# Kernel tuning notes

Hardware: AMD Instinct MI355X
Metric: run time of the kernel (lower is better)

The kernel has to match this reference:

```python
import jax, jax.numpy as jnp
import numpy as np

B, S, C, P = 1024, 336, 321, 96  # batch, seq_len, input_dim, pred_len


def setup_inputs() -> dict:
    key = jax.random.key(0)
    kx, kw, kb = jax.random.split(key, 3)
    x = jax.random.normal(kx, (B, S, C), dtype=jnp.float32)
    # per-channel Linear(seq_len -> pred_len): W[c] is [P, S], b[c] is [P]
    W = jax.random.normal(kw, (C, P, S), dtype=jnp.float32) * (1.0 / np.sqrt(S))
    b = jax.random.normal(kb, (C, P), dtype=jnp.float32) * 0.01
    return {"x": x, "W": W, "b": b}


def reference(x, W, b):
    # x: [B, S, C]
    seq_last = x[:, -1:, :]                      # [B, 1, C] (detached in torch; values identical)
    xn = x - seq_last                            # subtract last-step normalization
    # per-channel linear: out[b,c,p] = sum_s W[c,p,s] * xn[b,s,c] + b[c,p]
    out = jnp.einsum("bsc,cps->bcp", xn, W) + b  # [B, C, P]
    out = out.transpose(0, 2, 1) + seq_last      # [B, P, C], add back last value
    return out[:, :, 3]                          # [B, P], channel-3 slice
```

## Files before the change

### kernel.cpp

```cpp
#include <hip/hip_runtime.h>


constexpr int B = 1024, S = 336, C = 321, P = 96;
constexpr int BPB   = 4;
constexpr int BLOCK = 256;

__global__ __launch_bounds__(BLOCK) void nlinear_c3_kernel(
    const float* __restrict__ x, const float* __restrict__ W,
    const float* __restrict__ bias, float* __restrict__ out)
{
    __shared__ float xs[BPB][S];

    const int b0 = blockIdx.x * BPB;

    for (int idx = threadIdx.x; idx < BPB * S; idx += BLOCK) {
        const int bi = idx / S;
        const int s  = idx - bi * S;
        xs[bi][s] = x[((size_t)(b0 + bi) * S + s) * C + 3];
    }
    __syncthreads();

    const int g = threadIdx.x >> 7;
    const int p = threadIdx.x & 127;
    if (p < P) {
        const int bA = 2 * g, bB = 2 * g + 1;
        const float lastA = xs[bA][S - 1];
        const float lastB = xs[bB][S - 1];

        const float4* __restrict__ wp4 =
            reinterpret_cast<const float4*>(W + (size_t)(3 * P + p) * S);
        const float4* xA4 = reinterpret_cast<const float4*>(xs[bA]);
        const float4* xB4 = reinterpret_cast<const float4*>(xs[bB]);

        float accA = 0.f, accB = 0.f, sw = 0.f;
        #pragma unroll 4
        for (int i = 0; i < S / 4; ++i) {
            const float4 w  = wp4[i];
            const float4 a  = xA4[i];
            const float4 c  = xB4[i];
            accA += a.x * w.x + a.y * w.y + a.z * w.z + a.w * w.w;
            accB += c.x * w.x + c.y * w.y + c.z * w.z + c.w * w.w;
            sw   += w.x + w.y + w.z + w.w;
        }

        const float bb = bias[3 * P + p];
        out[(size_t)(b0 + bA) * P + p] = accA - lastA * sw + bb + lastA;
        out[(size_t)(b0 + bB) * P + p] = accB - lastB * sw + bb + lastB;
    }
}

extern "C" void kernel_launch(void* const* d_in, const int* in_sizes, int n_in,
                              void* d_out, int out_size, void* d_ws, size_t ws_size,
                              hipStream_t stream) {
    const float* x    = (const float*)d_in[0];
    const float* W    = (const float*)d_in[1];
    const float* bias = (const float*)d_in[2];
    float* out        = (float*)d_out;

    nlinear_c3_kernel<<<B / BPB, BLOCK, 0, stream>>>(x, W, bias, out);
}
```

Measured before the change: 20.66 us.

## Use one block per batch row and split the reduction over four lanes

Each block now handles a single batch row with 384 threads. Four lanes share each output p, each taking a quarter of S, and their partial sums are combined with xor shuffles. The x gather uses nontemporal loads, and launch bounds request four blocks per CU. This raises parallelism and shortens the per-thread serial chain, but W reuse across batch rows inside a block drops from four to one, so W is read from cache more often.

Result: slower. 26.52 us (+28.4%).

```diff
diff --git a/kernel.cpp b/kernel.cpp
--- a/kernel.cpp
+++ b/kernel.cpp
@@ -2,50 +2,47 @@
 
 
 constexpr int B = 1024, S = 336, C = 321, P = 96;
-constexpr int BPB   = 4;
-constexpr int BLOCK = 256;
+constexpr int BLOCK = 384;
+constexpr int QCH = S / 4;
 
-__global__ __launch_bounds__(BLOCK) void nlinear_c3_kernel(
+__global__ __launch_bounds__(BLOCK, 4) void nlinear_c3_kernel(
     const float* __restrict__ x, const float* __restrict__ W,
     const float* __restrict__ bias, float* __restrict__ out)
 {
-    __shared__ float xs[BPB][S];
+    __shared__ float xs[S];
 
-    const int b0 = blockIdx.x * BPB;
+    const int b = blockIdx.x;
+    const int t = threadIdx.x;
 
-    for (int idx = threadIdx.x; idx < BPB * S; idx += BLOCK) {
-        const int bi = idx / S;
-        const int s  = idx - bi * S;
-        xs[bi][s] = x[((size_t)(b0 + bi) * S + s) * C + 3];
+    if (t < S) {
+        xs[t] = __builtin_nontemporal_load(&x[((size_t)b * S + t) * C + 3]);
     }
     __syncthreads();
 
-    const int g = threadIdx.x >> 7;
-    const int p = threadIdx.x & 127;
-    if (p < P) {
-        const int bA = 2 * g, bB = 2 * g + 1;
-        const float lastA = xs[bA][S - 1];
-        const float lastB = xs[bB][S - 1];
+    const int p = t >> 2;
+    const int q = t & 3;
 
-        const float4* __restrict__ wp4 =
-            reinterpret_cast<const float4*>(W + (size_t)(3 * P + p) * S);
-        const float4* xA4 = reinterpret_cast<const float4*>(xs[bA]);
-        const float4* xB4 = reinterpret_cast<const float4*>(xs[bB]);
+    const float last = xs[S - 1];
 
-        float accA = 0.f, accB = 0.f, sw = 0.f;
-        #pragma unroll 4
-        for (int i = 0; i < S / 4; ++i) {
-            const float4 w  = wp4[i];
-            const float4 a  = xA4[i];
-            const float4 c  = xB4[i];
-            accA += a.x * w.x + a.y * w.y + a.z * w.z + a.w * w.w;
-            accB += c.x * w.x + c.y * w.y + c.z * w.z + c.w * w.w;
-            sw   += w.x + w.y + w.z + w.w;
-        }
+    const float4* __restrict__ wp4 =
+        reinterpret_cast<const float4*>(W + (size_t)(3 * P + p) * S + q * QCH);
+    const float4* __restrict__ xq4 =
+        reinterpret_cast<const float4*>(xs + q * QCH);
 
-        const float bb = bias[3 * P + p];
-        out[(size_t)(b0 + bA) * P + p] = accA - lastA * sw + bb + lastA;
-        out[(size_t)(b0 + bB) * P + p] = accB - lastB * sw + bb + lastB;
+    float acc = 0.f, sw = 0.f;
+    #pragma unroll 7
+    for (int i = 0; i < QCH / 4; ++i) {
+        const float4 w = wp4[i];
+        const float4 a = xq4[i];
+        acc += a.x * w.x + a.y * w.y + a.z * w.z + a.w * w.w;
+        sw  += w.x + w.y + w.z + w.w;
+    }
+
+    acc += __shfl_xor(acc, 1);  sw += __shfl_xor(sw, 1);
+    acc += __shfl_xor(acc, 2);  sw += __shfl_xor(sw, 2);
+
+    if (q == 0) {
+        out[(size_t)b * P + p] = acc - last * sw + bias[3 * P + p] + last;
     }
 }
 
@@ -57,5 +54,5 @@
     const float* bias = (const float*)d_in[2];
     float* out        = (float*)d_out;
 
-    nlinear_c3_kernel<<<B / BPB, BLOCK, 0, stream>>>(x, W, bias, out);
+    nlinear_c3_kernel<<<B, BLOCK, 0, stream>>>(x, W, bias, out);
 }
```

## Split channel-3 gather into a separate kernel and read gathered x from workspace

Applied to the files above, without the earlier changes.

Replaces the single fused kernel with two launches. The first gathers the strided channel-3 column of x into a contiguous workspace buffer using many small blocks, so more gather parallelism is exposed. The second computes the per-row dot products straight from global memory using 192-thread blocks with no idle lanes and no shared memory or barrier. The trade-off is an extra kernel launch and a round trip through global memory for the gathered data.

After: 22.98 us. 11.2% more time.

```diff
diff --git a/kernel.cpp b/kernel.cpp
--- a/kernel.cpp
+++ b/kernel.cpp
@@ -2,51 +2,59 @@
 
 
 constexpr int B = 1024, S = 336, C = 321, P = 96;
-constexpr int BPB   = 4;
-constexpr int BLOCK = 256;
+constexpr int TOTAL = B * S;
 
-__global__ __launch_bounds__(BLOCK) void nlinear_c3_kernel(
-    const float* __restrict__ x, const float* __restrict__ W,
+constexpr int GBLOCK = 256;
+constexpr int GELEMS = 2;
+constexpr int GGRID  = TOTAL / (GBLOCK * GELEMS);
+
+__global__ __launch_bounds__(GBLOCK) void gather_c3(
+    const float* __restrict__ x, float* __restrict__ g)
+{
+    const int base = blockIdx.x * (GBLOCK * GELEMS) + threadIdx.x;
+    const float v0 = x[(size_t)base * C + 3];
+    const float v1 = x[(size_t)(base + GBLOCK) * C + 3];
+    g[base]          = v0;
+    g[base + GBLOCK] = v1;
+}
+
+constexpr int CBLOCK = 192;
+constexpr int BPB    = 4;
+constexpr int CGRID  = B / BPB;
+
+__global__ __launch_bounds__(CBLOCK) void dot_c3(
+    const float* __restrict__ g, const float* __restrict__ W,
     const float* __restrict__ bias, float* __restrict__ out)
 {
-    __shared__ float xs[BPB][S];
+    const int t   = threadIdx.x;
+    const int grp = t / 96;
+    const int p   = t - grp * 96;
+    const int bA  = blockIdx.x * BPB + 2 * grp;
+    const int bB  = bA + 1;
 
-    const int b0 = blockIdx.x * BPB;
+    const float4* __restrict__ wp4 =
+        reinterpret_cast<const float4*>(W + (size_t)(3 * P + p) * S);
+    const float4* __restrict__ xA4 =
+        reinterpret_cast<const float4*>(g + (size_t)bA * S);
+    const float4* __restrict__ xB4 =
+        reinterpret_cast<const float4*>(g + (size_t)bB * S);
 
-    for (int idx = threadIdx.x; idx < BPB * S; idx += BLOCK) {
-        const int bi = idx / S;
-        const int s  = idx - bi * S;
-        xs[bi][s] = x[((size_t)(b0 + bi) * S + s) * C + 3];
+    float accA = 0.f, accB = 0.f, sw = 0.f;
+    #pragma unroll 4
+    for (int i = 0; i < S / 4; ++i) {
+        const float4 w = wp4[i];
+        const float4 a = xA4[i];
+        const float4 c = xB4[i];
+        accA += a.x * w.x + a.y * w.y + a.z * w.z + a.w * w.w;
+        accB += c.x * w.x + c.y * w.y + c.z * w.z + c.w * w.w;
+        sw   += w.x + w.y + w.z + w.w;
     }
-    __syncthreads();
 
-    const int g = threadIdx.x >> 7;
-    const int p = threadIdx.x & 127;
-    if (p < P) {
-        const int bA = 2 * g, bB = 2 * g + 1;
-        const float lastA = xs[bA][S - 1];
-        const float lastB = xs[bB][S - 1];
-
-        const float4* __restrict__ wp4 =
-            reinterpret_cast<const float4*>(W + (size_t)(3 * P + p) * S);
-        const float4* xA4 = reinterpret_cast<const float4*>(xs[bA]);
-        const float4* xB4 = reinterpret_cast<const float4*>(xs[bB]);
-
-        float accA = 0.f, accB = 0.f, sw = 0.f;
-        #pragma unroll 4
-        for (int i = 0; i < S / 4; ++i) {
-            const float4 w  = wp4[i];
-            const float4 a  = xA4[i];
-            const float4 c  = xB4[i];
-            accA += a.x * w.x + a.y * w.y + a.z * w.z + a.w * w.w;
-            accB += c.x * w.x + c.y * w.y + c.z * w.z + c.w * w.w;
-            sw   += w.x + w.y + w.z + w.w;
-        }
-
-        const float bb = bias[3 * P + p];
-        out[(size_t)(b0 + bA) * P + p] = accA - lastA * sw + bb + lastA;
-        out[(size_t)(b0 + bB) * P + p] = accB - lastB * sw + bb + lastB;
-    }
+    const float lastA = g[(size_t)bA * S + (S - 1)];
+    const float lastB = g[(size_t)bB * S + (S - 1)];
+    const float bb    = bias[3 * P + p];
+    out[(size_t)bA * P + p] = accA - lastA * sw + bb + lastA;
+    out[(size_t)bB * P + p] = accB - lastB * sw + bb + lastB;
 }
 
 extern "C" void kernel_launch(void* const* d_in, const int* in_sizes, int n_in,
@@ -56,6 +64,8 @@
     const float* W    = (const float*)d_in[1];
     const float* bias = (const float*)d_in[2];
     float* out        = (float*)d_out;
+    float* g          = (float*)d_ws;
 
-    nlinear_c3_kernel<<<B / BPB, BLOCK, 0, stream>>>(x, W, bias, out);
+    gather_c3<<<GGRID, GBLOCK, 0, stream>>>(x, g);
+    dot_c3<<<CGRID, CBLOCK, 0, stream>>>(g, W, bias, out);
 }
```
